# Kernel optimization log

Hardware: AMD Instinct MI355X
Metric: run time of the kernel (lower is better)

Reference implementation:

```python
import jax, jax.numpy as jnp
import numpy as np

THR = 0.2
TEMPERATURE = 0.1


def setup_inputs() -> dict:
    key = jax.random.key(0)
    k0, k1 = jax.random.split(key)
    N, L, S, C = 4, 4096, 4096, 256
    feat_c0 = jax.random.normal(k0, (N, L, C), dtype=jnp.float32)
    feat_c1 = jax.random.normal(k1, (N, S, C), dtype=jnp.float32)
    return {"feat_c0": feat_c0, "feat_c1": feat_c1}


def reference(feat_c0, feat_c1):
    C = feat_c0.shape[-1]
    scale = 1.0 / (float(C) ** 0.5)
    f0 = feat_c0 * scale  # [N, L, C]
    f1 = feat_c1 * scale  # [N, S, C]

    # sim_matrix = -cdist(f0, f1) / temperature / C  (Euclidean distance)
    sq0 = jnp.sum(f0 * f0, axis=-1)  # [N, L]
    sq1 = jnp.sum(f1 * f1, axis=-1)  # [N, S]
    inner = jnp.einsum('nlc,nsc->nls', f0, f1)  # [N, L, S]
    d2 = jnp.maximum(sq0[:, :, None] + sq1[:, None, :] - 2.0 * inner, 0.0)
    dist = jnp.sqrt(d2)
    sim_matrix = -dist / (TEMPERATURE * C)

    # dual softmax
    conf_matrix0 = jax.nn.softmax(sim_matrix, axis=1)
    conf_matrix1 = jax.nn.softmax(sim_matrix, axis=2)
    conf_matrix = conf_matrix0 * conf_matrix1

    # mutual-nearest-neighbor + threshold matching (dense, jit-friendly form)
    mask = conf_matrix > THR
    i_mask = conf_matrix == jnp.max(conf_matrix, axis=2, keepdims=True)
    j_mask = conf_matrix == jnp.max(conf_matrix, axis=1, keepdims=True)
    mask = mask & i_mask & j_mask  # [N, L, S]

    mask_v = jnp.any(mask, axis=2)                  # [N, L] — row i has a match
    all_j_ids = jnp.argmax(mask, axis=2)            # [N, L] — matched column j
    mconf = jnp.take_along_axis(conf_matrix, all_j_ids[:, :, None], axis=2)[:, :, 0]
    mconf = jnp.where(mask_v, mconf, 0.0)           # [N, L] dense match confidence

    return (conf_matrix, conf_matrix0, conf_matrix1, sim_matrix,
            mask_v, all_j_ids, mconf)
```

## Files before the change

kernel.cpp:

```cpp
#include <hip/hip_runtime.h>
#include <stdint.h>

#define NB 4
#define LD 4096
#define SD 4096
#define CD 256

static constexpr long CHUNK = (long)NB * LD * SD;
static constexpr float SCALE = 0.0625f;
static constexpr float INV_TC = 1.0f / 25.6f;
static constexpr float THRV = 0.2f;

typedef __attribute__((ext_vector_type(8))) short bf16x8;
typedef __attribute__((ext_vector_type(4))) float f32x4;

__device__ __forceinline__ unsigned short f2bf(float x) {
  unsigned int u = __float_as_uint(x);
  return (unsigned short)((u + 0x7FFFu + ((u >> 16) & 1u)) >> 16);
}

__device__ __forceinline__ void gload_lds16(const void* g, void* l) {
  __builtin_amdgcn_global_load_lds((const __attribute__((address_space(1))) void*)g,
                                   (__attribute__((address_space(3))) void*)l, 16, 0, 0);
}

__global__ __launch_bounds__(256) void k_prep(const float* __restrict__ f0,
                                              const float* __restrict__ f1,
                                              unsigned short* __restrict__ abf,
                                              unsigned short* __restrict__ bbf,
                                              float* __restrict__ sq0,
                                              float* __restrict__ sq1) {
  int wid = threadIdx.x >> 6, lane = threadIdx.x & 63;
  long row = (long)blockIdx.x * 4 + wid;
  const long nl = (long)NB * LD;
  const float* src;
  unsigned short* dst;
  float* sqd;
  if (row < nl) {
    src = f0 + row * CD; dst = abf + row * CD; sqd = sq0 + row;
  } else {
    long r = row - nl;
    src = f1 + r * CD; dst = bbf + r * CD; sqd = sq1 + r;
  }
  float4 v = reinterpret_cast<const float4*>(src)[lane];
  v.x *= SCALE; v.y *= SCALE; v.z *= SCALE; v.w *= SCALE;
  ushort4 o;
  o.x = f2bf(v.x); o.y = f2bf(v.y); o.z = f2bf(v.z); o.w = f2bf(v.w);
  reinterpret_cast<ushort4*>(dst)[lane] = o;
  float s = v.x * v.x + v.y * v.y + v.z * v.z + v.w * v.w;
  #pragma unroll
  for (int m = 1; m < 64; m <<= 1) s += __shfl_xor(s, m);
  if (lane == 0) *sqd = s;
}

__device__ __forceinline__ void gemm_core(const char* aB, const char* bB, char* lds,
                                          int t, f32x4 (&acc)[4][4]) {
  int wid = t >> 6, lane = t & 63;
  int srow = t >> 3;
  int scolb = (t & 7) << 4;
  int wrb = (wid >> 1) << 6;
  int wcb = (wid & 1) << 6;
  int lrow = lane & 15;
  int kgrp = lane >> 4;

  #pragma unroll
  for (int m = 0; m < 4; ++m)
    #pragma unroll
    for (int n = 0; n < 4; ++n)
      acc[m][n] = (f32x4){0.f, 0.f, 0.f, 0.f};

  for (int kt = 0; kt < 4; ++kt) {
    #pragma unroll
    for (int i = 0; i < 4; ++i) {
      int row = i * 32 + srow;
      int sc = scolb ^ ((row & 7) << 4);
      gload_lds16(aB + (long)row * (CD * 2) + kt * 128 + sc,
                  lds + i * 4096 + (wid << 10));
      gload_lds16(bB + (long)row * (CD * 2) + kt * 128 + sc,
                  lds + 16384 + i * 4096 + (wid << 10));
    }
    __syncthreads();
    #pragma unroll
    for (int ks = 0; ks < 2; ++ks) {
      int kb = ks * 64 + kgrp * 16;
      bf16x8 af[4], bfr[4];
      #pragma unroll
      for (int m = 0; m < 4; ++m) {
        int r = wrb + m * 16 + lrow;
        af[m] = *(const bf16x8*)(lds + r * 128 + (kb ^ ((r & 7) << 4)));
      }
      #pragma unroll
      for (int n = 0; n < 4; ++n) {
        int r = wcb + n * 16 + lrow;
        bfr[n] = *(const bf16x8*)(lds + 16384 + r * 128 + (kb ^ ((r & 7) << 4)));
      }
      #pragma unroll
      for (int m = 0; m < 4; ++m)
        #pragma unroll
        for (int n = 0; n < 4; ++n)
          acc[m][n] = __builtin_amdgcn_mfma_f32_16x16x32_bf16(af[m], bfr[n], acc[m][n], 0, 0, 0);
    }
    __syncthreads();
  }
}

__global__ __launch_bounds__(256) void k_gemm(const unsigned short* __restrict__ abf,
                                              const unsigned short* __restrict__ bbf,
                                              const float* __restrict__ sq0,
                                              const float* __restrict__ sq1,
                                              float* __restrict__ simout,
                                              float* __restrict__ rowsum,
                                              float* __restrict__ colsum) {
  __shared__ char lds[33792];
  int t = threadIdx.x;
  int wid = t >> 6, lane = t & 63;
  int wrb = (wid >> 1) << 6, wcb = (wid & 1) << 6;
  int lrow = lane & 15, kgrp = lane >> 4;
  int bz = blockIdx.z;
  long tileM = (long)blockIdx.y * 128;
  long tileS = (long)blockIdx.x * 128;
  const char* aB = (const char*)(abf + ((long)bz * LD + tileM) * CD);
  const char* bB = (const char*)(bbf + ((long)bz * SD + tileS) * CD);

  f32x4 acc[4][4];
  gemm_core(aB, bB, lds, t, acc);

  long gcol0 = (long)bz * SD + tileS + wcb;
  float sq1v[4];
  #pragma unroll
  for (int n = 0; n < 4; ++n) sq1v[n] = sq1[gcol0 + n * 16 + lrow];

  float ce[4] = {0.f, 0.f, 0.f, 0.f};
  float* ltile = (float*)lds;

  #pragma unroll
  for (int h = 0; h < 2; ++h) {
    __syncthreads();
    #pragma unroll
    for (int mm = 0; mm < 2; ++mm) {
      int m = 2 * h + mm;
      #pragma unroll
      for (int i = 0; i < 4; ++i) {
        int lr = m * 16 + kgrp * 4 + i;
        long gl = tileM + wrb + lr;
        float s0 = sq0[(long)bz * LD + gl];
        int q = (wid >> 1) * 32 + mm * 16 + kgrp * 4 + i;
        float rs = 0.f;
        #pragma unroll
        for (int n = 0; n < 4; ++n) {
          float inner = acc[m][n][i];
          float d2 = fmaxf(s0 + sq1v[n] - 2.0f * inner, 0.f);
          float sv = -__builtin_sqrtf(d2) * INV_TC;
          ltile[q * 132 + wcb + n * 16 + lrow] = sv;
          float e = __expf(sv);
          rs += e;
          ce[n] += e;
        }
        #pragma unroll
        for (int d = 1; d < 16; d <<= 1) rs += __shfl_xor(rs, d);
        if (lrow == 0) atomicAdd(&rowsum[(long)bz * LD + gl], rs);
      }
    }
    __syncthreads();
    #pragma unroll
    for (int j = 0; j < 8; ++j) {
      int f = t + 256 * j;
      int r = f >> 5;
      int c4 = f & 31;
      long grow = tileM + (r >> 5) * 64 + 32 * h + (r & 31);
      float4 v = *(const float4*)&ltile[r * 132 + c4 * 4];
      *(float4*)(simout + ((long)bz * LD + grow) * SD + tileS + c4 * 4) = v;
    }
  }

  #pragma unroll
  for (int n = 0; n < 4; ++n) {
    float cs = ce[n];
    cs += __shfl_xor(cs, 16);
    cs += __shfl_xor(cs, 32);
    if (kgrp == 0) atomicAdd(&colsum[gcol0 + n * 16 + lrow], cs);
  }
}

__global__ __launch_bounds__(256) void k_softmax(const float* __restrict__ sim,
                                                 const float* __restrict__ rowsum,
                                                 const float* __restrict__ colsum,
                                                 float* __restrict__ conf,
                                                 float* __restrict__ conf0,
                                                 float* __restrict__ conf1,
                                                 unsigned long long* __restrict__ rowpack,
                                                 unsigned long long* __restrict__ colpack) {
  __shared__ unsigned long long rmx[64];
  __shared__ unsigned long long cmx[512];
  int t = threadIdx.x;
  if (t < 64) rmx[t] = 0ull;
  cmx[t] = 0ull;
  cmx[t + 256] = 0ull;
  __syncthreads();

  int n = blockIdx.z;
  long rbase = (long)blockIdx.y * 64;
  long cbase = (long)blockIdx.x * 512;
  int c4 = t & 127;
  int rpar = t >> 7;
  long col0 = cbase + (long)c4 * 4;

  f32x4 csv = *(const f32x4*)(colsum + (long)n * SD + col0);
  f32x4 invc;
  invc[0] = 1.0f / csv[0]; invc[1] = 1.0f / csv[1];
  invc[2] = 1.0f / csv[2]; invc[3] = 1.0f / csv[3];

  unsigned long long cpk[4] = {0ull, 0ull, 0ull, 0ull};

  for (int j = 0; j < 32; ++j) {
    int r = rpar + j * 2;
    long gr = rbase + r;
    float invr = 1.0f / rowsum[(long)n * LD + gr];
    long idx = ((long)n * LD + gr) * SD + col0;
    f32x4 sv = *(const f32x4*)(sim + idx);
    f32x4 cf, c0v, c1v;
    unsigned long long best = 0ull;
    #pragma unroll
    for (int q = 0; q < 4; ++q) {
      float e = __expf(sv[q]);
      float a0 = e * invc[q];
      float a1 = e * invr;
      float c = a0 * a1;
      c0v[q] = a0; c1v[q] = a1; cf[q] = c;
      unsigned long long pk = ((unsigned long long)__float_as_uint(c) << 32) |
                              (unsigned int)(~(unsigned int)(col0 + q));
      best = pk > best ? pk : best;
      cpk[q] = pk > cpk[q] ? pk : cpk[q];
    }
    *(f32x4*)(conf + idx) = cf;
    *(f32x4*)(conf0 + idx) = c0v;
    *(f32x4*)(conf1 + idx) = c1v;
    #pragma unroll
    for (int d = 1; d < 64; d <<= 1) {
      unsigned long long o = __shfl_xor(best, d);
      best = o > best ? o : best;
    }
    if ((t & 63) == 0) atomicMax(&rmx[r], best);
  }
  #pragma unroll
  for (int q = 0; q < 4; ++q) atomicMax(&cmx[c4 * 4 + q], cpk[q]);
  __syncthreads();
  if (t < 64) atomicMax(&rowpack[(long)n * LD + rbase + t], rmx[t]);
  atomicMax(&colpack[(long)n * SD + cbase + t], cmx[t]);
  atomicMax(&colpack[(long)n * SD + cbase + 256 + t], cmx[t + 256]);
}

__global__ __launch_bounds__(256) void k_final(const unsigned long long* __restrict__ rowpack,
                                               const unsigned long long* __restrict__ colpack,
                                               float* __restrict__ maskv,
                                               float* __restrict__ jids,
                                               float* __restrict__ mconf) {
  long idx = (long)blockIdx.x * 256 + threadIdx.x;
  if (idx >= (long)NB * LD) return;
  int n = (int)(idx / LD);
  unsigned long long rp = rowpack[idx];
  unsigned int cbits = (unsigned int)(rp >> 32);
  float cval = __uint_as_float(cbits);
  unsigned int col = ~(unsigned int)rp;
  bool valid = (cval > THRV) && (col < (unsigned int)SD);
  if (valid) {
    unsigned long long cp = colpack[(long)n * SD + col];
    valid = ((unsigned int)(cp >> 32)) == cbits;
  }
  maskv[idx] = valid ? 1.0f : 0.0f;
  jids[idx]  = valid ? (float)col : 0.0f;
  mconf[idx] = valid ? cval : 0.0f;
}

extern "C" void kernel_launch(void* const* d_in, const int* in_sizes, int n_in,
                              void* d_out, int out_size, void* d_ws, size_t ws_size,
                              hipStream_t stream) {
  const float* f0 = (const float*)d_in[0];
  const float* f1 = (const float*)d_in[1];
  float* out = (float*)d_out;
  float* conf  = out;
  float* conf0 = out + CHUNK;
  float* conf1 = out + 2 * CHUNK;
  float* simo  = out + 3 * CHUNK;
  float* maskv = out + 4 * CHUNK;
  float* jids  = maskv + (long)NB * LD;
  float* mconf = jids + (long)NB * LD;

  char* ws = (char*)d_ws;
  unsigned short* abf = (unsigned short*)ws;
  unsigned short* bbf = (unsigned short*)(ws + 8388608);
  float* sq0 = (float*)(ws + 16777216);
  float* sq1 = (float*)(ws + 16777216 + 65536);
  char* accums = ws + 16908288;
  float* rowsum = (float*)accums;
  float* colsum = (float*)(accums + 65536);
  unsigned long long* rowpack = (unsigned long long*)(accums + 131072);
  unsigned long long* colpack = (unsigned long long*)(accums + 262144);
  hipMemsetAsync(accums, 0, 393216, stream);

  k_prep<<<dim3((NB * (LD + SD)) / 4), dim3(256), 0, stream>>>(f0, f1, abf, bbf, sq0, sq1);
  k_gemm<<<dim3(SD / 128, LD / 128, NB), dim3(256), 0, stream>>>(abf, bbf, sq0, sq1,
                                                                 simo, rowsum, colsum);
  k_softmax<<<dim3(SD / 512, LD / 64, NB), dim3(256), 0, stream>>>(simo, rowsum, colsum,
                                                                   conf, conf0, conf1,
                                                                   rowpack, colpack);
  k_final<<<dim3((NB * LD + 255) / 256), dim3(256), 0, stream>>>(rowpack, colpack,
                                                                 maskv, jids, mconf);
}
```

Before: 390.6 us.

## Use nontemporal stores/loads, XCD-aware GEMM tile swizzle, and wave-per-row softmax

Large sim/conf outputs are now written and read with nontemporal stores and loads to avoid polluting cache. The GEMM grid is flattened to 1D and remapped so that consecutive workgroups on each XCD share nearby tiles. The softmax kernel now assigns one wave per row, so the row max is computed inside a single wave and written without an LDS atomic. There is some risk that nontemporal loads of sim, which was just written, lose L2 hits.

After: 392.3 us. No clear change (+0.4%).

```diff
diff --git a/kernel.cpp b/kernel.cpp
--- a/kernel.cpp
+++ b/kernel.cpp
@@ -22,6 +22,13 @@
 __device__ __forceinline__ void gload_lds16(const void* g, void* l) {
   __builtin_amdgcn_global_load_lds((const __attribute__((address_space(1))) void*)g,
                                    (__attribute__((address_space(3))) void*)l, 16, 0, 0);
+}
+
+__device__ __forceinline__ void nt_store4(f32x4 v, float* p) {
+  __builtin_nontemporal_store(v, (f32x4*)p);
+}
+__device__ __forceinline__ f32x4 nt_load4(const float* p) {
+  return __builtin_nontemporal_load((const f32x4*)p);
 }
 
 __global__ __launch_bounds__(256) void k_prep(const float* __restrict__ f0,
@@ -42,12 +49,12 @@
     long r = row - nl;
     src = f1 + r * CD; dst = bbf + r * CD; sqd = sq1 + r;
   }
-  float4 v = reinterpret_cast<const float4*>(src)[lane];
-  v.x *= SCALE; v.y *= SCALE; v.z *= SCALE; v.w *= SCALE;
+  f32x4 v = *reinterpret_cast<const f32x4*>(src + lane * 4);
+  v *= SCALE;
   ushort4 o;
-  o.x = f2bf(v.x); o.y = f2bf(v.y); o.z = f2bf(v.z); o.w = f2bf(v.w);
+  o.x = f2bf(v[0]); o.y = f2bf(v[1]); o.z = f2bf(v[2]); o.w = f2bf(v[3]);
   reinterpret_cast<ushort4*>(dst)[lane] = o;
-  float s = v.x * v.x + v.y * v.y + v.z * v.z + v.w * v.w;
+  float s = v[0] * v[0] + v[1] * v[1] + v[2] * v[2] + v[3] * v[3];
   #pragma unroll
   for (int m = 1; m < 64; m <<= 1) s += __shfl_xor(s, m);
   if (lane == 0) *sqd = s;
@@ -116,9 +123,13 @@
   int wid = t >> 6, lane = t & 63;
   int wrb = (wid >> 1) << 6, wcb = (wid & 1) << 6;
   int lrow = lane & 15, kgrp = lane >> 4;
-  int bz = blockIdx.z;
-  long tileM = (long)blockIdx.y * 128;
-  long tileS = (long)blockIdx.x * 128;
+
+  int wg = blockIdx.x;
+  int swz = (wg & 7) * 512 + (wg >> 3);
+  int bz = swz >> 10;
+  int rem = swz & 1023;
+  long tileM = (long)(rem >> 5) * 128;
+  long tileS = (long)(rem & 31) * 128;
   const char* aB = (const char*)(abf + ((long)bz * LD + tileM) * CD);
   const char* bB = (const char*)(bbf + ((long)bz * SD + tileS) * CD);
 
@@ -168,8 +179,8 @@
       int r = f >> 5;
       int c4 = f & 31;
       long grow = tileM + (r >> 5) * 64 + 32 * h + (r & 31);
-      float4 v = *(const float4*)&ltile[r * 132 + c4 * 4];
-      *(float4*)(simout + ((long)bz * LD + grow) * SD + tileS + c4 * 4) = v;
+      f32x4 v = *(const f32x4*)&ltile[r * 132 + c4 * 4];
+      nt_store4(v, simout + ((long)bz * LD + grow) * SD + tileS + c4 * 4);
     }
   }
 
@@ -193,7 +204,7 @@
   __shared__ unsigned long long rmx[64];
   __shared__ unsigned long long cmx[512];
   int t = threadIdx.x;
-  if (t < 64) rmx[t] = 0ull;
+  int w = t >> 6, lane = t & 63;
   cmx[t] = 0ull;
   cmx[t + 256] = 0ull;
   __syncthreads();
@@ -201,49 +212,59 @@
   int n = blockIdx.z;
   long rbase = (long)blockIdx.y * 64;
   long cbase = (long)blockIdx.x * 512;
-  int c4 = t & 127;
-  int rpar = t >> 7;
-  long col0 = cbase + (long)c4 * 4;
-
-  f32x4 csv = *(const f32x4*)(colsum + (long)n * SD + col0);
-  f32x4 invc;
-  invc[0] = 1.0f / csv[0]; invc[1] = 1.0f / csv[1];
-  invc[2] = 1.0f / csv[2]; invc[3] = 1.0f / csv[3];
-
-  unsigned long long cpk[4] = {0ull, 0ull, 0ull, 0ull};
-
-  for (int j = 0; j < 32; ++j) {
-    int r = rpar + j * 2;
+
+  float invc[2][4];
+  unsigned long long cpk[2][4];
+  #pragma unroll
+  for (int it = 0; it < 2; ++it) {
+    f32x4 cs = *(const f32x4*)(colsum + (long)n * SD + cbase + it * 256 + lane * 4);
+    invc[it][0] = 1.0f / cs[0]; invc[it][1] = 1.0f / cs[1];
+    invc[it][2] = 1.0f / cs[2]; invc[it][3] = 1.0f / cs[3];
+    cpk[it][0] = cpk[it][1] = cpk[it][2] = cpk[it][3] = 0ull;
+  }
+
+  #pragma unroll 2
+  for (int j = 0; j < 16; ++j) {
+    int r = w + j * 4;
     long gr = rbase + r;
     float invr = 1.0f / rowsum[(long)n * LD + gr];
-    long idx = ((long)n * LD + gr) * SD + col0;
-    f32x4 sv = *(const f32x4*)(sim + idx);
-    f32x4 cf, c0v, c1v;
-    unsigned long long best = 0ull;
-    #pragma unroll
-    for (int q = 0; q < 4; ++q) {
-      float e = __expf(sv[q]);
-      float a0 = e * invc[q];
-      float a1 = e * invr;
-      float c = a0 * a1;
-      c0v[q] = a0; c1v[q] = a1; cf[q] = c;
-      unsigned long long pk = ((unsigned long long)__float_as_uint(c) << 32) |
-                              (unsigned int)(~(unsigned int)(col0 + q));
-      best = pk > best ? pk : best;
-      cpk[q] = pk > cpk[q] ? pk : cpk[q];
-    }
-    *(f32x4*)(conf + idx) = cf;
-    *(f32x4*)(conf0 + idx) = c0v;
-    *(f32x4*)(conf1 + idx) = c1v;
+    long rowoff = ((long)n * LD + gr) * SD + cbase;
+    unsigned long long rbest = 0ull;
+    #pragma unroll
+    for (int it = 0; it < 2; ++it) {
+      long idx = rowoff + it * 256 + lane * 4;
+      f32x4 sv = nt_load4(sim + idx);
+      f32x4 cf, c0v, c1v;
+      #pragma unroll
+      for (int q = 0; q < 4; ++q) {
+        float e = __expf(sv[q]);
+        float a0 = e * invc[it][q];
+        float a1 = e * invr;
+        float c = a0 * a1;
+        c0v[q] = a0;
+        c1v[q] = a1;
+        cf[q] = c;
+        unsigned long long pk = ((unsigned long long)__float_as_uint(c) << 32) |
+                                (unsigned int)(~(unsigned int)(cbase + it * 256 + lane * 4 + q));
+        rbest = pk > rbest ? pk : rbest;
+        cpk[it][q] = pk > cpk[it][q] ? pk : cpk[it][q];
+      }
+      nt_store4(cf, conf + idx);
+      nt_store4(c0v, conf0 + idx);
+      nt_store4(c1v, conf1 + idx);
+    }
     #pragma unroll
     for (int d = 1; d < 64; d <<= 1) {
-      unsigned long long o = __shfl_xor(best, d);
-      best = o > best ? o : best;
-    }
-    if ((t & 63) == 0) atomicMax(&rmx[r], best);
-  }
-  #pragma unroll
-  for (int q = 0; q < 4; ++q) atomicMax(&cmx[c4 * 4 + q], cpk[q]);
+      unsigned long long o = __shfl_xor(rbest, d);
+      rbest = o > rbest ? o : rbest;
+    }
+    if (lane == 0) rmx[r] = rbest;
+  }
+  #pragma unroll
+  for (int it = 0; it < 2; ++it)
+    #pragma unroll
+    for (int q = 0; q < 4; ++q)
+      atomicMax(&cmx[it * 256 + lane * 4 + q], cpk[it][q]);
   __syncthreads();
   if (t < 64) atomicMax(&rowpack[(long)n * LD + rbase + t], rmx[t]);
   atomicMax(&colpack[(long)n * SD + cbase + t], cmx[t]);
@@ -296,11 +317,10 @@
   float* colsum = (float*)(accums + 65536);
   unsigned long long* rowpack = (unsigned long long*)(accums + 131072);
   unsigned long long* colpack = (unsigned long long*)(accums + 262144);
-  hipMemsetAsync(accums, 0, 393216, stream);
+  (void)hipMemsetAsync(accums, 0, 393216, stream);
 
   k_prep<<<dim3((NB * (LD + SD)) / 4), dim3(256), 0, stream>>>(f0, f1, abf, bbf, sq0, sq1);
-  k_gemm<<<dim3(SD / 128, LD / 128, NB), dim3(256), 0, stream>>>(abf, bbf, sq0, sq1,
-                                                                 simo, rowsum, colsum);
+  k_gemm<<<dim3(4096), dim3(256), 0, stream>>>(abf, bbf, sq0, sq1, simo, rowsum, colsum);
   k_softmax<<<dim3(SD / 512, LD / 64, NB), dim3(256), 0, stream>>>(simo, rowsum, colsum,
                                                                    conf, conf0, conf1,
                                                                    rowpack, colpack);
```
